# Kernel optimization log

Hardware: AMD Instinct MI355X
Metric: run time of the kernel (lower is better)

Reference implementation:

```python
import jax, jax.numpy as jnp
import numpy as np


def setup_inputs() -> dict:
    key = jax.random.key(0)
    ks = jax.random.split(key, 13)
    B, T, D, H, E, C, S = 256, 64, 512, 512, 256, 6624, 26
    s = 0.05
    return {
        "batch_H": jax.random.normal(ks[0], (B, T, D), jnp.float32),
        "text": jax.random.randint(ks[1], (B, S), 0, C, jnp.int64),
        "W_i2h": jax.random.normal(ks[2], (H, D), jnp.float32) * s,
        "W_h2h": jax.random.normal(ks[3], (H, H), jnp.float32) * s,
        "b_h2h": jax.random.normal(ks[4], (H,), jnp.float32) * s,
        "w_score": jax.random.normal(ks[5], (H,), jnp.float32) * s,
        "W_ih": jax.random.normal(ks[6], (4 * H, D + E), jnp.float32) * s,
        "W_hh": jax.random.normal(ks[7], (4 * H, H), jnp.float32) * s,
        "b_ih": jax.random.normal(ks[8], (4 * H,), jnp.float32) * s,
        "b_hh": jax.random.normal(ks[9], (4 * H,), jnp.float32) * s,
        "emb": jax.random.normal(ks[10], (C, E), jnp.float32) * s,
        "W_gen": jax.random.normal(ks[11], (C, H), jnp.float32) * s,
        "b_gen": jax.random.normal(ks[12], (C,), jnp.float32) * s,
        "max_label_length": 25,
    }


def reference(batch_H, text, W_i2h, W_h2h, b_h2h, w_score, W_ih, W_hh,
              b_ih, b_hh, emb, W_gen, b_gen, max_label_length):
    B, T, D = batch_H.shape
    H = W_h2h.shape[0]
    num_steps = max_label_length + 1

    # i2h(batch_H) is constant across steps -> hoist out of the recurrence
    Hproj = jnp.einsum('btd,hd->bth', batch_H, W_i2h)  # [B,T,H]
    char_embs = emb[text[:, :num_steps]]               # [B,S,E]
    xs = jnp.transpose(char_embs, (1, 0, 2))           # [S,B,E]

    def step(carry, ce):
        h, c = carry
        hp = h @ W_h2h.T + b_h2h                       # [B,H]
        e = jnp.tanh(Hproj + hp[:, None, :]) @ w_score  # [B,T]
        alpha = jax.nn.softmax(e, axis=1)
        context = jnp.einsum('bt,btd->bd', alpha, batch_H)  # [B,D]
        x = jnp.concatenate([context, ce], axis=1)     # [B,D+E]
        gates = x @ W_ih.T + b_ih + h @ W_hh.T + b_hh  # [B,4H]
        i, f, g, o = jnp.split(gates, 4, axis=1)
        c_new = jax.nn.sigmoid(f) * c + jax.nn.sigmoid(i) * jnp.tanh(g)
        h_new = jax.nn.sigmoid(o) * jnp.tanh(c_new)
        return (h_new, c_new), h_new

    h0 = jnp.zeros((B, H), batch_H.dtype)
    c0 = jnp.zeros((B, H), batch_H.dtype)
    _, hs = jax.lax.scan(step, (h0, c0), xs)           # hs: [S,B,H]
    output_hiddens = jnp.transpose(hs, (1, 0, 2))      # [B,S,H]
    probs = output_hiddens @ W_gen.T + b_gen           # [B,S,C]
    return probs
```

## Files before the change

kernel.cpp:

```cpp
#include <hip/hip_runtime.h>

typedef unsigned short u16;
typedef unsigned int   u32;
typedef __attribute__((ext_vector_type(2))) float f32x2;
typedef __attribute__((ext_vector_type(4))) float f32x4;
typedef __attribute__((ext_vector_type(8))) u16   u16x8;
typedef __attribute__((ext_vector_type(4))) u16   u16x4;
typedef __attribute__((ext_vector_type(4))) u32   u32x4;

__device__ __forceinline__ u16 f2bf(float x) {
  u32 u = __builtin_bit_cast(u32, x);
  u = (u + 0x7fffu + ((u >> 16) & 1u)) >> 16;
  return (u16)u;
}
__device__ __forceinline__ float bf2f(u16 h) {
  return __builtin_bit_cast(float, (u32)h << 16);
}
__device__ __forceinline__ float fast_sig(float x) { return 1.f / (1.f + __expf(-x)); }
__device__ __forceinline__ float fast_tanh(float x) {
  float e = __expf(2.f * x);
  return 1.f - 2.f / (e + 1.f);
}

__device__ __forceinline__ f32x4 mfma_bf16(u16x8 a, u16x8 b, f32x4 c) {
  asm volatile("v_mfma_f32_16x16x32_bf16 %0, %1, %2, %0" : "+v"(c) : "v"(a), "v"(b));
  return c;
}

__device__ __forceinline__ void gload_lds16(const void* g, void* l) {
  __builtin_amdgcn_global_load_lds(
      (__attribute__((address_space(1))) u32*)g,
      (__attribute__((address_space(3))) u32*)l, 16, 0, 0);
}

__device__ __forceinline__ void conv4(const float* __restrict__ s, u16* __restrict__ d, int i) {
  f32x4 v = *(const f32x4*)(s + i);
  u16x4 o;
  o.x = f2bf(v.x); o.y = f2bf(v.y); o.z = f2bf(v.z); o.w = f2bf(v.w);
  *(u16x4*)(d + i) = o;
}

__global__ __launch_bounds__(256) void k_prep(
    const float* __restrict__ batch_H, const float* __restrict__ W_i2h,
    const float* __restrict__ emb, const float* __restrict__ W_ih,
    const float* __restrict__ W_h2h, const float* __restrict__ W_hh,
    const float* __restrict__ W_gen, const float* __restrict__ b_ih,
    const float* __restrict__ b_hh, const float* __restrict__ b_h2h,
    u16* __restrict__ bHb, u16* __restrict__ Wi2hb, u16* __restrict__ embb,
    u16* __restrict__ Wctxb, u16* __restrict__ Wceb, u16* __restrict__ Whcatb,
    u16* __restrict__ Wgenb, float* __restrict__ biascat,
    u16* __restrict__ hb, float* __restrict__ cst,
    float* __restrict__ hpbuf, float* __restrict__ ghbuf) {
  const u32 u = blockIdx.x * 256 + threadIdx.x;
  if (u < 2097152u) { conv4(batch_H, bHb, u * 4); return; }
  if (u < 2162688u) { conv4(W_i2h, Wi2hb, (u - 2097152u) * 4); return; }
  if (u < 2586624u) { conv4(emb, embb, (u - 2162688u) * 4); return; }
  if (u < 2588672u) {
    *(u16x4*)(embb + 1695744u + (u - 2586624u) * 4) = (u16x4){0, 0, 0, 0};
    return;
  }
  if (u < 2850816u) {
    int i = (u - 2588672u) * 4;
    int r = i >> 9, c = i & 511;
    f32x4 v = *(const f32x4*)(W_ih + (size_t)r * 768 + c);
    u16x4 o;
    o.x = f2bf(v.x); o.y = f2bf(v.y); o.z = f2bf(v.z); o.w = f2bf(v.w);
    *(u16x4*)(Wctxb + i) = o;
    return;
  }
  if (u < 2981888u) {
    int i = (u - 2850816u) * 4;
    int r = i >> 8, c = i & 255;
    f32x4 v = *(const f32x4*)(W_ih + (size_t)r * 768 + 512 + c);
    u16x4 o;
    o.x = f2bf(v.x); o.y = f2bf(v.y); o.z = f2bf(v.z); o.w = f2bf(v.w);
    *(u16x4*)(Wceb + i) = o;
    return;
  }
  if (u < 3309568u) {
    int i = (u - 2981888u) * 4;
    int r = i >> 9, c = i & 511;
    const float* src = (r < 512) ? (W_h2h + (size_t)r * 512 + c)
                                 : (W_hh + (size_t)(r - 512) * 512 + c);
    f32x4 v = *(const f32x4*)src;
    u16x4 o;
    o.x = f2bf(v.x); o.y = f2bf(v.y); o.z = f2bf(v.z); o.w = f2bf(v.w);
    *(u16x4*)(Whcatb + i) = o;
    return;
  }
  if (u < 4161536u) {
    int i = (u - 3309568u) * 4;
    int r = i >> 9;
    if (r < 6624) conv4(W_gen, Wgenb, i);
    else *(u16x4*)(Wgenb + i) = (u16x4){0, 0, 0, 0};
    return;
  }
  if (u < 4162048u) {
    int j = (u - 4161536u) * 4;
    f32x4 a = *(const f32x4*)(b_ih + j), b = *(const f32x4*)(b_hh + j);
    f32x4 r = {a.x + b.x, a.y + b.y, a.z + b.z, a.w + b.w};
    *(f32x4*)(biascat + j) = r;
    return;
  }
  if (u < 4178432u) {
    *(u32x4*)((char*)hb + (size_t)(u - 4162048u) * 16) = (u32x4){0, 0, 0, 0};
    return;
  }
  if (u < 4211200u) {
    *(u32x4*)((char*)cst + (size_t)(u - 4178432u) * 16) = (u32x4){0, 0, 0, 0};
    return;
  }
  if (u < 4243968u) {
    int i = (u - 4211200u) * 4;
    int j = i & 511;
    *(f32x4*)(hpbuf + i) = *(const f32x4*)(b_h2h + j);
    return;
  }
  if (u < 4375040u) {
    *(u32x4*)((char*)ghbuf + (size_t)(u - 4243968u) * 16) = (u32x4){0, 0, 0, 0};
    return;
  }
}

template <int OUT_MODE>
__device__ __forceinline__ void gemm128_body(
    const u16* __restrict__ A, int lda, const u16* __restrict__ B, int ldb,
    const float* __restrict__ bias, float* __restrict__ Cf, u16* __restrict__ Cb,
    int ldc, int Nreal, int K, int m0, int n0, char* smem) {
  u16* sA = (u16*)smem;
  u16* sB = (u16*)(smem + 32768);
  const int tid = threadIdx.x;
  const int lane = tid & 63, wave = tid >> 6;
  const int wr = wave >> 1, wc = wave & 1;
  const int l15 = lane & 15, lhi = lane >> 4;

  f32x4 acc[4][4];
#pragma unroll
  for (int i = 0; i < 4; ++i)
#pragma unroll
    for (int j = 0; j < 4; ++j) acc[i][j] = 0.f;

  for (int k0 = 0; k0 < K; k0 += 128) {
    __syncthreads();
#pragma unroll
    for (int j = 0; j < 8; ++j) {
      int idx = j * 256 + tid, row = idx >> 4, cc = idx & 15, c = cc ^ (row & 15);
      gload_lds16(A + (size_t)(m0 + row) * lda + (k0 + c * 8), sA + idx * 8);
    }
#pragma unroll
    for (int j = 0; j < 8; ++j) {
      int idx = j * 256 + tid, row = idx >> 4, cc = idx & 15, c = cc ^ (row & 15);
      gload_lds16(B + (size_t)(n0 + row) * ldb + (k0 + c * 8), sB + idx * 8);
    }
    __syncthreads();

#pragma unroll
    for (int ks = 0; ks < 4; ++ks) {
      u16x8 av[4], bv[4];
#pragma unroll
      for (int mi = 0; mi < 4; ++mi) {
        int row = wr * 64 + mi * 16 + l15;
        int ch = row * 16 + ((ks * 4 + lhi) ^ (row & 15));
        av[mi] = *(const u16x8*)(sA + ch * 8);
      }
#pragma unroll
      for (int ni = 0; ni < 4; ++ni) {
        int row = wc * 64 + ni * 16 + l15;
        int ch = row * 16 + ((ks * 4 + lhi) ^ (row & 15));
        bv[ni] = *(const u16x8*)(sB + ch * 8);
      }
#pragma unroll
      for (int mi = 0; mi < 4; ++mi)
#pragma unroll
        for (int ni = 0; ni < 4; ++ni) acc[mi][ni] = mfma_bf16(av[mi], bv[ni], acc[mi][ni]);
    }
  }

  asm volatile("s_nop 7\ns_nop 7\ns_nop 7");

#pragma unroll
  for (int mi = 0; mi < 4; ++mi) {
#pragma unroll
    for (int ni = 0; ni < 4; ++ni) {
      int col = n0 + wc * 64 + ni * 16 + l15;
      if (col < Nreal) {
        float bvv = (OUT_MODE == 1 || OUT_MODE == 3) ? bias[col] : 0.f;
#pragma unroll
        for (int r = 0; r < 4; ++r) {
          int row = m0 + wr * 64 + mi * 16 + lhi * 4 + r;
          float v = acc[mi][ni][r] + bvv;
          if (OUT_MODE == 2 || OUT_MODE == 3)
            Cb[(size_t)row * ldc + col] = f2bf(v);
          else
            Cf[(size_t)row * ldc + col] = v;
        }
      }
    }
  }
}

template <int OUT_MODE, bool SWZ>
__global__ __launch_bounds__(256) void kGemm128(const u16* __restrict__ A, int lda,
                                                const u16* __restrict__ B, int ldb,
                                                const float* __restrict__ bias,
                                                float* __restrict__ Cf, u16* __restrict__ Cb,
                                                int ldc, int Nreal, int K) {
  __shared__ __align__(16) char smem[65536];
  int bx = blockIdx.x, by = blockIdx.y;
  if (SWZ) {
    int gx = gridDim.x;
    int lin = by * gx + bx;
    int q = (gx * gridDim.y) >> 3;
    int idx = (lin & 7) * q + (lin >> 3);
    by = idx / gx;
    bx = idx - by * gx;
  }
  gemm128_body<OUT_MODE>(A, lda, B, ldb, bias, Cf, Cb, ldc, Nreal, K,
                         by * 128, bx * 128, smem);
}

__global__ __launch_bounds__(256) void kHE(const u16* __restrict__ bHb,
                                           const u16* __restrict__ Wi2hb,
                                           u16* __restrict__ Hproj,
                                           const u16* __restrict__ embb,
                                           const u16* __restrict__ Wceb,
                                           const float* __restrict__ biascat,
                                           u16* __restrict__ E2Gb) {
  __shared__ __align__(16) char smem[65536];
  const int bid = blockIdx.x;
  if (bid < 512) {
    gemm128_body<2>(bHb, 512, Wi2hb, 512, nullptr, nullptr, Hproj, 512, 512, 512,
                    (bid >> 2) * 128, (bid & 3) * 128, smem);
  } else {
    int r = bid - 512;
    gemm128_body<3>(embb, 256, Wceb, 256, biascat, nullptr, E2Gb, 2048, 2048, 256,
                    (r >> 4) * 128, (r & 15) * 128, smem);
  }
}

__global__ __launch_bounds__(256) void kA_hpgh(const u16* __restrict__ hb,
                                               const u16* __restrict__ Whcatb,
                                               const float* __restrict__ b_h2h,
                                               float* __restrict__ hpbuf,
                                               float* __restrict__ ghbuf) {
  extern __shared__ __align__(16) char smem[];
  u16* sA = (u16*)smem;
  u16* sB = (u16*)(smem + 65536);
  const int tid = threadIdx.x;
  const int lane = tid & 63, wave = tid >> 6;
  const int l15 = lane & 15, lhi = lane >> 4;
  const int b0 = ((int)blockIdx.x / 40) * 64, n0 = ((int)blockIdx.x % 40) * 64;

#pragma unroll
  for (int j = 0; j < 16; ++j) {
    int idx = j * 256 + tid, row = idx >> 6, cc = idx & 63, c = cc ^ (row & 15);
    gload_lds16(hb + (size_t)(b0 + row) * 512 + c * 8, sA + idx * 8);
  }
#pragma unroll
  for (int j = 0; j < 16; ++j) {
    int idx = j * 256 + tid, row = idx >> 6, cc = idx & 63, c = cc ^ (row & 15);
    gload_lds16(Whcatb + (size_t)(n0 + row) * 512 + c * 8, sB + idx * 8);
  }
  __syncthreads();

  f32x4 acc[4];
#pragma unroll
  for (int j = 0; j < 4; ++j) acc[j] = 0.f;
#pragma unroll
  for (int ks = 0; ks < 16; ++ks) {
    u16x8 av, bv[4];
    {
      int row = wave * 16 + l15;
      int ch = row * 64 + ((ks * 4 + lhi) ^ (row & 15));
      av = *(const u16x8*)(sA + ch * 8);
    }
#pragma unroll
    for (int ni = 0; ni < 4; ++ni) {
      int row = ni * 16 + l15;
      int ch = row * 64 + ((ks * 4 + lhi) ^ (row & 15));
      bv[ni] = *(const u16x8*)(sB + ch * 8);
    }
#pragma unroll
    for (int ni = 0; ni < 4; ++ni) acc[ni] = mfma_bf16(av, bv[ni], acc[ni]);
  }
  asm volatile("s_nop 7\ns_nop 7\ns_nop 7");
#pragma unroll
  for (int ni = 0; ni < 4; ++ni) {
    int col = n0 + ni * 16 + l15;
    int rowg = b0 + wave * 16 + lhi * 4;
    if (col < 512) {
      float bvv = b_h2h[col];
#pragma unroll
      for (int r = 0; r < 4; ++r)
        hpbuf[(size_t)(rowg + r) * 512 + col] = acc[ni][r] + bvv;
    } else {
#pragma unroll
      for (int r = 0; r < 4; ++r)
        ghbuf[(size_t)(rowg + r) * 2048 + col - 512] = acc[ni][r];
    }
  }
}

__global__ __launch_bounds__(256) void kB_attn(const u16* __restrict__ Hproj,
                                               const float* __restrict__ hpbuf,
                                               const float* __restrict__ wsc,
                                               const u16* __restrict__ bh,
                                               u16* __restrict__ ctxb) {
  const int b = blockIdx.x, tid = threadIdx.x;
  __shared__ float hpsp[528];
  __shared__ float wssp[528];
  __shared__ float es[64];

  {
    int j0 = tid * 2;
    hpsp[j0 + (j0 >> 5)] = hpbuf[(size_t)b * 512 + j0];
    hpsp[j0 + 1 + ((j0 + 1) >> 5)] = hpbuf[(size_t)b * 512 + j0 + 1];
    int pi = j0 + (j0 >> 5);
    wssp[pi] = wsc[j0];
    wssp[pi + 1] = wsc[j0 + 1];
  }
  __syncthreads();

  const int ch16 = tid & 15;
  const int hbase = ch16 * 33;
  const int hc = ch16 * 32;
  float hpr[32], wsr[32];
#pragma unroll
  for (int j = 0; j < 32; ++j) {
    hpr[j] = hpsp[hbase + j];
    wsr[j] = wssp[hbase + j];
  }
#pragma unroll
  for (int tg = 0; tg < 4; ++tg) {
    int t = tg * 16 + (tid >> 4);
    const u16* hr = Hproj + (size_t)(b * 64 + t) * 512 + hc;
    float s = 0.f;
#pragma unroll
    for (int jo = 0; jo < 32; jo += 8) {
      u16x8 hv = *(const u16x8*)(hr + jo);
#pragma unroll
      for (int j = 0; j < 8; ++j) {
        float x = bf2f(hv[j]) + hpr[jo + j];
        s += fast_tanh(x) * wsr[jo + j];
      }
    }
#pragma unroll
    for (int off = 8; off; off >>= 1) s += __shfl_xor(s, off, 16);
    if (ch16 == 0) es[t] = s;
  }
  __syncthreads();
  if (tid < 64) {
    float v = es[tid];
    float m = v;
#pragma unroll
    for (int o = 32; o; o >>= 1) m = fmaxf(m, __shfl_xor(m, o, 64));
    float p = __expf(v - m);
    float su = p;
#pragma unroll
    for (int o = 32; o; o >>= 1) su += __shfl_xor(su, o, 64);
    es[tid] = p / su;
  }
  __syncthreads();
  const u16* base = bh + (size_t)b * 32768 + tid * 2;
  float c0 = 0.f, c1 = 0.f;
#pragma unroll 8
  for (int t = 0; t < 64; ++t) {
    u32 w = *(const u32*)(base + t * 512);
    float a = es[t];
    c0 = fmaf(a, bf2f((u16)(w & 0xffffu)), c0);
    c1 = fmaf(a, bf2f((u16)(w >> 16)), c1);
  }
  u32 pk = (u32)f2bf(c0) | ((u32)f2bf(c1) << 16);
  *(u32*)(ctxb + (size_t)b * 512 + tid * 2) = pk;
}

__global__ __launch_bounds__(256) void kC_gates_lstm(const u16* __restrict__ ctxb,
                                                     const u16* __restrict__ Wctxb,
                                                     const u16* __restrict__ E2Gb,
                                                     const float* __restrict__ ghbuf,
                                                     const int* __restrict__ text,
                                                     float* __restrict__ cst,
                                                     u16* __restrict__ hb,
                                                     u16* __restrict__ hsb, int step) {
  extern __shared__ __align__(16) char smem[];
  u16* sA = (u16*)smem;
  u16* sB = (u16*)(smem + 32768);
  const int tid = threadIdx.x;
  const int lane = tid & 63, wave = tid >> 6;
  const int wr = wave >> 1, wc = wave & 1;
  const int l15 = lane & 15, lhi = lane >> 4;
  const int jj = blockIdx.x;
  const int b0 = blockIdx.y * 32;

#pragma unroll
  for (int j = 0; j < 8; ++j) {
    int idx = j * 256 + tid, row = idx >> 6, cc = idx & 63, c = cc ^ (row & 15);
    gload_lds16(ctxb + (size_t)(b0 + row) * 512 + c * 8, sA + idx * 8);
  }
#pragma unroll
  for (int j = 0; j < 16; ++j) {
    int idx = j * 256 + tid, row = idx >> 6, cc = idx & 63, c = cc ^ (row & 15);
    int grow = (row >> 4) * 512 + jj * 16 + (row & 15);
    gload_lds16(Wctxb + (size_t)grow * 512 + c * 8, sB + idx * 8);
  }
  __syncthreads();

  f32x4 acc[2];
#pragma unroll
  for (int j = 0; j < 2; ++j) acc[j] = 0.f;
#pragma unroll
  for (int ks = 0; ks < 16; ++ks) {
    u16x8 av, bv[2];
    {
      int row = wr * 16 + l15;
      int ch = row * 64 + ((ks * 4 + lhi) ^ (row & 15));
      av = *(const u16x8*)(sA + ch * 8);
    }
#pragma unroll
    for (int ni = 0; ni < 2; ++ni) {
      int row = wc * 32 + ni * 16 + l15;
      int ch = row * 64 + ((ks * 4 + lhi) ^ (row & 15));
      bv[ni] = *(const u16x8*)(sB + ch * 8);
    }
#pragma unroll
    for (int ni = 0; ni < 2; ++ni) acc[ni] = mfma_bf16(av, bv[ni], acc[ni]);
  }

  asm volatile("s_nop 7\ns_nop 7\ns_nop 7");
  __syncthreads();
  float (*gsm)[68] = (float(*)[68])smem;
#pragma unroll
  for (int ni = 0; ni < 2; ++ni) {
    int col = wc * 32 + ni * 16 + l15;
    int row = wr * 16 + lhi * 4;
#pragma unroll
    for (int r = 0; r < 4; ++r) gsm[row + r][col] = acc[ni][r];
  }
  __syncthreads();

  {
    const int bl = tid >> 3, jl = (tid & 7) * 2;
    const int b = b0 + bl;
    const int jg = jj * 16 + jl;
    const int ci = text[b * 26 + step];
    const float* gh = ghbuf + (size_t)b * 2048;
    const u16* ge = E2Gb + (size_t)ci * 2048;
    float cn[2];
    u16 hbv[2];
#pragma unroll
    for (int q = 0; q < 2; ++q) {
      int jc = jl + q, j = jg + q;
      float gi = gsm[bl][jc]      + gh[j]        + bf2f(ge[j]);
      float gf = gsm[bl][16 + jc] + gh[512 + j]  + bf2f(ge[512 + j]);
      float gg = gsm[bl][32 + jc] + gh[1024 + j] + bf2f(ge[1024 + j]);
      float go = gsm[bl][48 + jc] + gh[1536 + j] + bf2f(ge[1536 + j]);
      float c = fast_sig(gf) * cst[(size_t)b * 512 + j] + fast_sig(gi) * fast_tanh(gg);
      cn[q] = c;
      hbv[q] = f2bf(fast_sig(go) * fast_tanh(c));
    }
    *(f32x2*)(cst + (size_t)b * 512 + jg) = *(f32x2*)cn;
    u32 pk = (u32)hbv[0] | ((u32)hbv[1] << 16);
    *(u32*)(hb + (size_t)b * 512 + jg) = pk;
    *(u32*)(hsb + (size_t)(b * 26 + step) * 512 + jg) = pk;
  }
}

extern "C" void kernel_launch(void* const* d_in, const int* in_sizes, int n_in,
                              void* d_out, int out_size, void* d_ws, size_t ws_size,
                              hipStream_t stream) {
  const float* batch_H = (const float*)d_in[0];
  const int*   text    = (const int*)d_in[1];
  const float* W_i2h   = (const float*)d_in[2];
  const float* W_h2h   = (const float*)d_in[3];
  const float* b_h2h   = (const float*)d_in[4];
  const float* w_score = (const float*)d_in[5];
  const float* W_ih    = (const float*)d_in[6];
  const float* W_hh    = (const float*)d_in[7];
  const float* b_ih    = (const float*)d_in[8];
  const float* b_hh    = (const float*)d_in[9];
  const float* emb     = (const float*)d_in[10];
  const float* W_gen   = (const float*)d_in[11];
  const float* b_gen   = (const float*)d_in[12];
  float* out = (float*)d_out;

  static bool attr_done = []() {
    hipFuncSetAttribute(reinterpret_cast<const void*>(kA_hpgh),
                        hipFuncAttributeMaxDynamicSharedMemorySize, 163840);
    hipFuncSetAttribute(reinterpret_cast<const void*>(kC_gates_lstm),
                        hipFuncAttributeMaxDynamicSharedMemorySize, 163840);
    return true;
  }();
  (void)attr_done;

  u16* bHb   = (u16*)d_out;
  u16* Hproj = bHb + 8388608;

  char* w = (char*)d_ws;
  auto alloc = [&](size_t bytes) {
    char* p = w;
    w += (bytes + 255) & ~(size_t)255;
    return p;
  };
  u16*   Wi2hb   = (u16*)alloc(512ull * 512 * 2);
  u16*   Whcatb  = (u16*)alloc(2560ull * 512 * 2);
  u16*   Wctxb   = (u16*)alloc(2048ull * 512 * 2);
  u16*   Wceb    = (u16*)alloc(2048ull * 256 * 2);
  u16*   Wgenb   = (u16*)alloc(6656ull * 512 * 2);
  u16*   embb    = (u16*)alloc(6656ull * 256 * 2);
  float* biascat = (float*)alloc(2048ull * 4);
  u16*   ctxb    = (u16*)alloc(256ull * 512 * 2);
  u16*   hb      = (u16*)alloc(256ull * 512 * 2);
  float* cst     = (float*)alloc(256ull * 512 * 4);
  float* hpbuf   = (float*)alloc(256ull * 512 * 4);
  float* ghbuf   = (float*)alloc(256ull * 2048 * 4);
  u16*   hsb     = (u16*)alloc(6656ull * 512 * 2);
  u16*   E2Gb    = (u16*)alloc(6656ull * 2048 * 2);

  k_prep<<<17090, 256, 0, stream>>>(batch_H, W_i2h, emb, W_ih, W_h2h, W_hh, W_gen,
                                    b_ih, b_hh, b_h2h, bHb, Wi2hb, embb, Wctxb, Wceb,
                                    Whcatb, Wgenb, biascat, hb, cst, hpbuf, ghbuf);

  kHE<<<1344, 256, 0, stream>>>(bHb, Wi2hb, Hproj, embb, Wceb, biascat, E2Gb);

  for (int s = 0; s < 26; ++s) {
    if (s > 0)
      kA_hpgh<<<160, 256, 131072, stream>>>(hb, Whcatb, b_h2h, hpbuf, ghbuf);
    kB_attn<<<256, 256, 0, stream>>>(Hproj, hpbuf, w_score, bHb, ctxb);
    kC_gates_lstm<<<dim3(32, 8), 256, 98304, stream>>>(ctxb, Wctxb, E2Gb, ghbuf, text,
                                                       cst, hb, hsb, s);
  }

  kGemm128<1, true><<<dim3(52, 52), 256, 0, stream>>>(
      hsb, 512, Wgenb, 512, b_gen, out, nullptr, 6624, 6624, 512);

  (void)in_sizes; (void)n_in; (void)out_size; (void)ws_size;
}
```

Before: 766.1 us.

## Fuse h2h projection into attention kernel and merge with hidden-gate GEMM launch

Merges the per-step hidden projection GEMM and the attention kernel into a single launch. 128 blocks compute h·W_h2h^T on CUDA cores from a pre-transposed bf16 copy, two batch rows per block, and then run the attention for those rows. The other 128 blocks compute the h·W_hh gate GEMM with MFMA. This removes one launch per step and the hpbuf round trip through global memory. In exchange each attention block re-reads the full 512x512 W_h2h from global or cache, and the projection now runs as scalar FMAs instead of MFMA.

```diff
diff --git a/kernel.cpp b/kernel.cpp
--- a/kernel.cpp
+++ b/kernel.cpp
@@ -45,12 +45,11 @@
     const float* __restrict__ emb, const float* __restrict__ W_ih,
     const float* __restrict__ W_h2h, const float* __restrict__ W_hh,
     const float* __restrict__ W_gen, const float* __restrict__ b_ih,
-    const float* __restrict__ b_hh, const float* __restrict__ b_h2h,
+    const float* __restrict__ b_hh,
     u16* __restrict__ bHb, u16* __restrict__ Wi2hb, u16* __restrict__ embb,
     u16* __restrict__ Wctxb, u16* __restrict__ Wceb, u16* __restrict__ Whcatb,
-    u16* __restrict__ Wgenb, float* __restrict__ biascat,
-    u16* __restrict__ hb, float* __restrict__ cst,
-    float* __restrict__ hpbuf, float* __restrict__ ghbuf) {
+    u16* __restrict__ Wgenb, float* __restrict__ biascat, u16* __restrict__ WTb,
+    u16* __restrict__ hb, float* __restrict__ cst) {
   const u32 u = blockIdx.x * 256 + threadIdx.x;
   if (u < 2097152u) { conv4(batch_H, bHb, u * 4); return; }
   if (u < 2162688u) { conv4(W_i2h, Wi2hb, (u - 2097152u) * 4); return; }
@@ -102,22 +101,21 @@
     *(f32x4*)(biascat + j) = r;
     return;
   }
-  if (u < 4178432u) {
-    *(u32x4*)((char*)hb + (size_t)(u - 4162048u) * 16) = (u32x4){0, 0, 0, 0};
-    return;
-  }
-  if (u < 4211200u) {
-    *(u32x4*)((char*)cst + (size_t)(u - 4178432u) * 16) = (u32x4){0, 0, 0, 0};
+  if (u < 4227584u) {
+    int i = (u - 4162048u) * 4;
+    int k = i >> 9, j = i & 511;
+    u16x4 o;
+#pragma unroll
+    for (int q = 0; q < 4; ++q) o[q] = f2bf(W_h2h[(size_t)(j + q) * 512 + k]);
+    *(u16x4*)(WTb + i) = o;
     return;
   }
   if (u < 4243968u) {
-    int i = (u - 4211200u) * 4;
-    int j = i & 511;
-    *(f32x4*)(hpbuf + i) = *(const f32x4*)(b_h2h + j);
-    return;
-  }
-  if (u < 4375040u) {
-    *(u32x4*)((char*)ghbuf + (size_t)(u - 4243968u) * 16) = (u32x4){0, 0, 0, 0};
+    *(u32x4*)((char*)hb + (size_t)(u - 4227584u) * 16) = (u32x4){0, 0, 0, 0};
+    return;
+  }
+  if (u < 4276736u) {
+    *(u32x4*)((char*)cst + (size_t)(u - 4243968u) * 16) = (u32x4){0, 0, 0, 0};
     return;
   }
 }
@@ -238,140 +236,177 @@
   }
 }
 
-__global__ __launch_bounds__(256) void kA_hpgh(const u16* __restrict__ hb,
-                                               const u16* __restrict__ Whcatb,
-                                               const float* __restrict__ b_h2h,
-                                               float* __restrict__ hpbuf,
-                                               float* __restrict__ ghbuf) {
+__global__ __launch_bounds__(256) void kBA(const u16* __restrict__ hb,
+                                           const u16* __restrict__ WTb,
+                                           const u16* __restrict__ Whcatb,
+                                           const float* __restrict__ b_h2h,
+                                           const float* __restrict__ wsc,
+                                           const u16* __restrict__ Hproj,
+                                           const u16* __restrict__ bh,
+                                           u16* __restrict__ ctxb,
+                                           float* __restrict__ ghbuf) {
   extern __shared__ __align__(16) char smem[];
-  u16* sA = (u16*)smem;
-  u16* sB = (u16*)(smem + 65536);
   const int tid = threadIdx.x;
-  const int lane = tid & 63, wave = tid >> 6;
-  const int l15 = lane & 15, lhi = lane >> 4;
-  const int b0 = ((int)blockIdx.x / 40) * 64, n0 = ((int)blockIdx.x % 40) * 64;
-
-#pragma unroll
-  for (int j = 0; j < 16; ++j) {
-    int idx = j * 256 + tid, row = idx >> 6, cc = idx & 63, c = cc ^ (row & 15);
-    gload_lds16(hb + (size_t)(b0 + row) * 512 + c * 8, sA + idx * 8);
-  }
-#pragma unroll
-  for (int j = 0; j < 16; ++j) {
-    int idx = j * 256 + tid, row = idx >> 6, cc = idx & 63, c = cc ^ (row & 15);
-    gload_lds16(Whcatb + (size_t)(n0 + row) * 512 + c * 8, sB + idx * 8);
-  }
-  __syncthreads();
-
-  f32x4 acc[4];
-#pragma unroll
-  for (int j = 0; j < 4; ++j) acc[j] = 0.f;
-#pragma unroll
-  for (int ks = 0; ks < 16; ++ks) {
-    u16x8 av, bv[4];
-    {
-      int row = wave * 16 + l15;
-      int ch = row * 64 + ((ks * 4 + lhi) ^ (row & 15));
-      av = *(const u16x8*)(sA + ch * 8);
-    }
+  const int bid = blockIdx.x;
+
+  if (bid >= 128) {
+    u16* sA = (u16*)smem;
+    u16* sB = (u16*)(smem + 65536);
+    const int r = bid - 128;
+    const int b0 = (r >> 5) * 64;
+    const int n0 = 512 + (r & 31) * 64;
+    const int lane = tid & 63, wave = tid >> 6;
+    const int l15 = lane & 15, lhi = lane >> 4;
+#pragma unroll
+    for (int j = 0; j < 16; ++j) {
+      int idx = j * 256 + tid, row = idx >> 6, cc = idx & 63, c = cc ^ (row & 15);
+      gload_lds16(hb + (size_t)(b0 + row) * 512 + c * 8, sA + idx * 8);
+    }
+#pragma unroll
+    for (int j = 0; j < 16; ++j) {
+      int idx = j * 256 + tid, row = idx >> 6, cc = idx & 63, c = cc ^ (row & 15);
+      gload_lds16(Whcatb + (size_t)(n0 + row) * 512 + c * 8, sB + idx * 8);
+    }
+    __syncthreads();
+
+    f32x4 acc[4];
+#pragma unroll
+    for (int j = 0; j < 4; ++j) acc[j] = 0.f;
+#pragma unroll
+    for (int ks = 0; ks < 16; ++ks) {
+      u16x8 av, bv[4];
+      {
+        int row = wave * 16 + l15;
+        int ch = row * 64 + ((ks * 4 + lhi) ^ (row & 15));
+        av = *(const u16x8*)(sA + ch * 8);
+      }
+#pragma unroll
+      for (int ni = 0; ni < 4; ++ni) {
+        int row = ni * 16 + l15;
+        int ch = row * 64 + ((ks * 4 + lhi) ^ (row & 15));
+        bv[ni] = *(const u16x8*)(sB + ch * 8);
+      }
+#pragma unroll
+      for (int ni = 0; ni < 4; ++ni) acc[ni] = mfma_bf16(av, bv[ni], acc[ni]);
+    }
+    asm volatile("s_nop 7\ns_nop 7\ns_nop 7");
 #pragma unroll
     for (int ni = 0; ni < 4; ++ni) {
-      int row = ni * 16 + l15;
-      int ch = row * 64 + ((ks * 4 + lhi) ^ (row & 15));
-      bv[ni] = *(const u16x8*)(sB + ch * 8);
-    }
-#pragma unroll
-    for (int ni = 0; ni < 4; ++ni) acc[ni] = mfma_bf16(av, bv[ni], acc[ni]);
-  }
-  asm volatile("s_nop 7\ns_nop 7\ns_nop 7");
-#pragma unroll
-  for (int ni = 0; ni < 4; ++ni) {
-    int col = n0 + ni * 16 + l15;
-    int rowg = b0 + wave * 16 + lhi * 4;
-    if (col < 512) {
-      float bvv = b_h2h[col];
-#pragma unroll
-      for (int r = 0; r < 4; ++r)
-        hpbuf[(size_t)(rowg + r) * 512 + col] = acc[ni][r] + bvv;
-    } else {
-#pragma unroll
-      for (int r = 0; r < 4; ++r)
-        ghbuf[(size_t)(rowg + r) * 2048 + col - 512] = acc[ni][r];
-    }
-  }
-}
-
-__global__ __launch_bounds__(256) void kB_attn(const u16* __restrict__ Hproj,
-                                               const float* __restrict__ hpbuf,
-                                               const float* __restrict__ wsc,
-                                               const u16* __restrict__ bh,
-                                               u16* __restrict__ ctxb) {
-  const int b = blockIdx.x, tid = threadIdx.x;
-  __shared__ float hpsp[528];
-  __shared__ float wssp[528];
-  __shared__ float es[64];
+      int col = n0 + ni * 16 + l15 - 512;
+      int rowg = b0 + wave * 16 + lhi * 4;
+#pragma unroll
+      for (int rr = 0; rr < 4; ++rr)
+        ghbuf[(size_t)(rowg + rr) * 2048 + col] = acc[ni][rr];
+    }
+    return;
+  }
+
+  float* hsm  = (float*)smem;
+  float* hpsp = (float*)(smem + 4096);
+  float* wssp = (float*)(smem + 8448);
+  float* es   = (float*)(smem + 10560);
+  const int b0 = bid * 2;
 
   {
+    int bb = tid >> 7, off = (tid & 127) * 4;
+    u16x4 hv = *(const u16x4*)(hb + (size_t)(b0 + bb) * 512 + off);
+#pragma unroll
+    for (int q = 0; q < 4; ++q) hsm[bb * 512 + off + q] = bf2f(hv[q]);
     int j0 = tid * 2;
-    hpsp[j0 + (j0 >> 5)] = hpbuf[(size_t)b * 512 + j0];
-    hpsp[j0 + 1 + ((j0 + 1) >> 5)] = hpbuf[(size_t)b * 512 + j0 + 1];
     int pi = j0 + (j0 >> 5);
     wssp[pi] = wsc[j0];
     wssp[pi + 1] = wsc[j0 + 1];
   }
   __syncthreads();
 
-  const int ch16 = tid & 15;
+  {
+    float a00 = 0.f, a01 = 0.f, a10 = 0.f, a11 = 0.f;
+    const u16* wp = WTb + tid * 2;
+#pragma unroll 8
+    for (int k = 0; k < 512; ++k) {
+      u32 ww = *(const u32*)(wp + (size_t)k * 512);
+      float f0 = bf2f((u16)(ww & 0xffffu)), f1 = bf2f((u16)(ww >> 16));
+      float h0 = hsm[k], h1 = hsm[512 + k];
+      a00 = fmaf(h0, f0, a00); a01 = fmaf(h0, f1, a01);
+      a10 = fmaf(h1, f0, a10); a11 = fmaf(h1, f1, a11);
+    }
+    int j0 = tid * 2, j1 = j0 + 1;
+    float bz0 = b_h2h[j0], bz1 = b_h2h[j1];
+    int p0 = j0 + (j0 >> 5), p1 = j1 + (j1 >> 5);
+    hpsp[p0] = a00 + bz0;
+    hpsp[p1] = a01 + bz1;
+    hpsp[528 + p0] = a10 + bz0;
+    hpsp[528 + p1] = a11 + bz1;
+  }
+  __syncthreads();
+
+  const int bb = tid >> 7, tid7 = tid & 127;
+  const int b = b0 + bb;
+  const int ch16 = tid7 & 15, trow = tid7 >> 4;
   const int hbase = ch16 * 33;
   const int hc = ch16 * 32;
-  float hpr[32], wsr[32];
-#pragma unroll
-  for (int j = 0; j < 32; ++j) {
-    hpr[j] = hpsp[hbase + j];
-    wsr[j] = wssp[hbase + j];
-  }
-#pragma unroll
-  for (int tg = 0; tg < 4; ++tg) {
-    int t = tg * 16 + (tid >> 4);
-    const u16* hr = Hproj + (size_t)(b * 64 + t) * 512 + hc;
-    float s = 0.f;
-#pragma unroll
-    for (int jo = 0; jo < 32; jo += 8) {
-      u16x8 hv = *(const u16x8*)(hr + jo);
-#pragma unroll
-      for (int j = 0; j < 8; ++j) {
-        float x = bf2f(hv[j]) + hpr[jo + j];
-        s += fast_tanh(x) * wsr[jo + j];
+  {
+    const float* hps = hpsp + bb * 528;
+    float hpr[32], wsr[32];
+#pragma unroll
+    for (int j = 0; j < 32; ++j) {
+      hpr[j] = hps[hbase + j];
+      wsr[j] = wssp[hbase + j];
+    }
+#pragma unroll
+    for (int tg = 0; tg < 8; ++tg) {
+      int t = tg * 8 + trow;
+      const u16* hr = Hproj + (size_t)(b * 64 + t) * 512 + hc;
+      float s = 0.f;
+#pragma unroll
+      for (int jo = 0; jo < 32; jo += 8) {
+        u16x8 hv = *(const u16x8*)(hr + jo);
+#pragma unroll
+        for (int j = 0; j < 8; ++j) {
+          float x = bf2f(hv[j]) + hpr[jo + j];
+          s += fast_tanh(x) * wsr[jo + j];
+        }
       }
-    }
-#pragma unroll
-    for (int off = 8; off; off >>= 1) s += __shfl_xor(s, off, 16);
-    if (ch16 == 0) es[t] = s;
-  }
-  __syncthreads();
-  if (tid < 64) {
-    float v = es[tid];
-    float m = v;
-#pragma unroll
-    for (int o = 32; o; o >>= 1) m = fmaxf(m, __shfl_xor(m, o, 64));
-    float p = __expf(v - m);
-    float su = p;
-#pragma unroll
-    for (int o = 32; o; o >>= 1) su += __shfl_xor(su, o, 64);
-    es[tid] = p / su;
-  }
-  __syncthreads();
-  const u16* base = bh + (size_t)b * 32768 + tid * 2;
-  float c0 = 0.f, c1 = 0.f;
+#pragma unroll
+      for (int off = 8; off; off >>= 1) s += __shfl_xor(s, off, 16);
+      if (ch16 == 0) es[bb * 64 + t] = s;
+    }
+  }
+  __syncthreads();
+  {
+    int wv = tid >> 6;
+    if ((wv & 1) == 0) {
+      int sb = wv >> 1, lane = tid & 63;
+      float v = es[sb * 64 + lane];
+      float m = v;
+#pragma unroll
+      for (int o = 32; o; o >>= 1) m = fmaxf(m, __shfl_xor(m, o, 64));
+      float p = __expf(v - m);
+      float su = p;
+#pragma unroll
+      for (int o = 32; o; o >>= 1) su += __shfl_xor(su, o, 64);
+      es[sb * 64 + lane] = p / su;
+    }
+  }
+  __syncthreads();
+  {
+    const int d0 = tid7 * 4;
+    const u16* base = bh + (size_t)b * 32768 + d0;
+    float c0 = 0.f, c1 = 0.f, c2 = 0.f, c3 = 0.f;
 #pragma unroll 8
-  for (int t = 0; t < 64; ++t) {
-    u32 w = *(const u32*)(base + t * 512);
-    float a = es[t];
-    c0 = fmaf(a, bf2f((u16)(w & 0xffffu)), c0);
-    c1 = fmaf(a, bf2f((u16)(w >> 16)), c1);
-  }
-  u32 pk = (u32)f2bf(c0) | ((u32)f2bf(c1) << 16);
-  *(u32*)(ctxb + (size_t)b * 512 + tid * 2) = pk;
+    for (int t = 0; t < 64; ++t) {
+      u32 w0 = *(const u32*)(base + t * 512);
+      u32 w1 = *(const u32*)(base + t * 512 + 2);
+      float a = es[bb * 64 + t];
+      c0 = fmaf(a, bf2f((u16)(w0 & 0xffffu)), c0);
+      c1 = fmaf(a, bf2f((u16)(w0 >> 16)), c1);
+      c2 = fmaf(a, bf2f((u16)(w1 & 0xffffu)), c2);
+      c3 = fmaf(a, bf2f((u16)(w1 >> 16)), c3);
+    }
+    u16x4 pk;
+    pk.x = f2bf(c0); pk.y = f2bf(c1); pk.z = f2bf(c2); pk.w = f2bf(c3);
+    *(u16x4*)(ctxb + (size_t)b * 512 + d0) = pk;
+  }
 }
 
 __global__ __launch_bounds__(256) void kC_gates_lstm(const u16* __restrict__ ctxb,
@@ -484,10 +519,10 @@
   float* out = (float*)d_out;
 
   static bool attr_done = []() {
-    hipFuncSetAttribute(reinterpret_cast<const void*>(kA_hpgh),
-                        hipFuncAttributeMaxDynamicSharedMemorySize, 163840);
+    hipFuncSetAttribute(reinterpret_cast<const void*>(kBA),
+                        hipFuncAttributeMaxDynamicSharedMemorySize, 131072);
     hipFuncSetAttribute(reinterpret_cast<const void*>(kC_gates_lstm),
-                        hipFuncAttributeMaxDynamicSharedMemorySize, 163840);
+                        hipFuncAttributeMaxDynamicSharedMemorySize, 98304);
     return true;
   }();
   (void)attr_done;
@@ -508,24 +543,23 @@
   u16*   Wgenb   = (u16*)alloc(6656ull * 512 * 2);
   u16*   embb    = (u16*)alloc(6656ull * 256 * 2);
   float* biascat = (float*)alloc(2048ull * 4);
+  u16*   WTb     = (u16*)alloc(512ull * 512 * 2);
   u16*   ctxb    = (u16*)alloc(256ull * 512 * 2);
   u16*   hb      = (u16*)alloc(256ull * 512 * 2);
   float* cst     = (float*)alloc(256ull * 512 * 4);
-  float* hpbuf   = (float*)alloc(256ull * 512 * 4);
   float* ghbuf   = (float*)alloc(256ull * 2048 * 4);
   u16*   hsb     = (u16*)alloc(6656ull * 512 * 2);
   u16*   E2Gb    = (u16*)alloc(6656ull * 2048 * 2);
 
-  k_prep<<<17090, 256, 0, stream>>>(batch_H, W_i2h, emb, W_ih, W_h2h, W_hh, W_gen,
-                                    b_ih, b_hh, b_h2h, bHb, Wi2hb, embb, Wctxb, Wceb,
-                                    Whcatb, Wgenb, biascat, hb, cst, hpbuf, ghbuf);
+  k_prep<<<16706, 256, 0, stream>>>(batch_H, W_i2h, emb, W_ih, W_h2h, W_hh, W_gen,
+                                    b_ih, b_hh, bHb, Wi2hb, embb, Wctxb, Wceb,
+                                    Whcatb, Wgenb, biascat, WTb, hb, cst);
 
   kHE<<<1344, 256, 0, stream>>>(bHb, Wi2hb, Hproj, embb, Wceb, biascat, E2Gb);
 
   for (int s = 0; s < 26; ++s) {
-    if (s > 0)
-      kA_hpgh<<<160, 256, 131072, stream>>>(hb, Whcatb, b_h2h, hpbuf, ghbuf);
-    kB_attn<<<256, 256, 0, stream>>>(Hproj, hpbuf, w_score, bHb, ctxb);
+    kBA<<<256, 256, 131072, stream>>>(hb, WTb, Whcatb, b_h2h, w_score, Hproj, bHb,
+                                      ctxb, ghbuf);
     kC_gates_lstm<<<dim3(32, 8), 256, 98304, stream>>>(ctxb, Wctxb, E2Gb, ghbuf, text,
                                                        cst, hb, hsb, s);
   }
```

New measurement: 1.292 ms. +68.7%, slower.
